# Optimization experiments

Hardware: AMD Instinct MI355X
Metric: run time of the kernel (lower is better)

## Reference

```python
import jax, jax.numpy as jnp
import numpy as np

D_HEAD = 64
SCALE = D_HEAD ** 0.5


def setup_inputs() -> dict:
    key = jax.random.key(0)
    kq, kk, kv = jax.random.split(key, 3)
    shape = (32, 2048, 64)  # (N = batch*heads, HW = seq, C = d_head)
    Q = jax.random.normal(kq, shape, dtype=jnp.float32)
    K = jax.random.normal(kk, shape, dtype=jnp.float32)
    V = jax.random.normal(kv, shape, dtype=jnp.float32)
    return {"Q": Q, "K": K, "V": V}


def reference(Q, K, V):
    # logits = Q K^T / sqrt(d_head); attn = softmax(logits); out = attn V
    logits = jnp.einsum('nqc,nkc->nqk', Q, K) / SCALE  # [N, HW, HW]
    attn = jax.nn.softmax(logits, axis=-1)
    return jnp.einsum('nqk,nkc->nqc', attn, V)  # [N, HW, C]
```

## Files before the change

### kernel.cpp

```cpp
#include <hip/hip_runtime.h>
#include <cstdint>
#include <cstddef>

typedef __bf16 bf16x8 __attribute__((ext_vector_type(8)));
typedef float f32x4 __attribute__((ext_vector_type(4)));
typedef float f32x16 __attribute__((ext_vector_type(16)));
typedef short s16x8 __attribute__((ext_vector_type(8)));
typedef unsigned short u16x4 __attribute__((ext_vector_type(4)));
typedef unsigned short u16x8 __attribute__((ext_vector_type(8)));
typedef int i32x4 __attribute__((ext_vector_type(4)));

#define S_LEN 2048
#define DH    64
#define BK    64
#define NTILE (S_LEN / BK)
#define NH    32

#if __has_builtin(__builtin_amdgcn_exp2f)
#define EXPF(x) __builtin_amdgcn_exp2f(x)
#define QSCALE 0.18033688011112043f
#else
#define EXPF(x) __expf(x)
#define QSCALE 0.125f
#endif

typedef const __attribute__((address_space(1))) void* gas_ptr;
typedef __attribute__((address_space(3))) void* las_ptr;

static __device__ __forceinline__ unsigned short f2bf(float x) {
    unsigned int u = __builtin_bit_cast(unsigned int, x);
    u += 0x7FFFu + ((u >> 16) & 1u);
    return (unsigned short)(u >> 16);
}

static __device__ __forceinline__ unsigned cvtpk(float lo, float hi) {
    unsigned r;
    asm("v_cvt_pk_bf16_f32 %0, %1, %2" : "=v"(r) : "v"(lo), "v"(hi));
    return r;
}

static __device__ __forceinline__ void swap32(int& x, int& y, int hi) {
#if __has_builtin(__builtin_amdgcn_permlane32_swap)
    (void)hi;
    auto r = __builtin_amdgcn_permlane32_swap(x, y, false, false);
    x = r[0]; y = r[1];
#else
    int px = __shfl_xor(x, 32), py = __shfl_xor(y, 32);
    int nx = hi ? py : x;
    int ny = hi ? y  : px;
    x = nx; y = ny;
#endif
}

static __device__ __forceinline__ bf16x8 mkfrag(int lo0, int lo1, int up0, int up1, int hi) {
    swap32(lo0, up0, hi);
    swap32(lo1, up1, hi);
    i32x4 f = {lo0, lo1, up0, up1};
    return __builtin_bit_cast(bf16x8, f);
}

__global__ __launch_bounds__(256) void prepass_kv(
        const float* __restrict__ K, const float* __restrict__ V,
        unsigned short* __restrict__ Kf, unsigned short* __restrict__ Vf)
{
    __shared__ float Tl[64][68];
    const int tid = threadIdx.x;
    const int head = blockIdx.x >> 5;
    const int tile = blockIdx.x & 31;

    const size_t hoff = (size_t)head * S_LEN * DH;
    const size_t soff = hoff + (size_t)tile * 64 * DH;

    #pragma unroll
    for (int p = 0; p < 4; ++p) {
        const int idx = p * 256 + tid;
        const int row = idx >> 4, c4 = idx & 15;
        *(float4*)&Tl[row][c4 * 4] = *(const float4*)(K + soff + (size_t)row * DH + c4 * 4);
    }
    __syncthreads();
    #pragma unroll
    for (int p = 0; p < 2; ++p) {
        const int cid = p * 256 + tid;
        const int sub = cid >> 6;
        const int ln  = cid & 63;
        const int dsub = sub >> 1, half = sub & 1;
        const int row  = half * 32 + (ln & 31);
        const int d0   = dsub * 16 + (ln >> 5) * 8;
        u16x8 o;
        #pragma unroll
        for (int e = 0; e < 8; ++e) o[e] = f2bf(Tl[row][d0 + e]);
        *(u16x8*)&Kf[hoff + (((size_t)tile * 8 + sub) * 64 + ln) * 8] = o;
    }
    __syncthreads();

    #pragma unroll
    for (int p = 0; p < 4; ++p) {
        const int idx = p * 256 + tid;
        const int row = idx >> 4, c4 = idx & 15;
        *(float4*)&Tl[row][c4 * 4] = *(const float4*)(V + soff + (size_t)row * DH + c4 * 4);
    }
    __syncthreads();
    #pragma unroll
    for (int p = 0; p < 2; ++p) {
        const int cid = p * 256 + tid;
        const int sub = cid >> 6;
        const int ln  = cid & 63;
        const int ks = sub >> 1, half = sub & 1;
        const int k0 = ks * 16 + (ln >> 5) * 8;
        const int d  = half * 32 + (ln & 31);
        u16x8 o;
        #pragma unroll
        for (int e = 0; e < 8; ++e) o[e] = f2bf(Tl[k0 + e][d]);
        *(u16x8*)&Vf[hoff + (((size_t)tile * 8 + sub) * 64 + ln) * 8] = o;
    }
}

__global__ __launch_bounds__(512, 4) void sdpa_fused(
        const float* __restrict__ Qg, const unsigned short* __restrict__ Kf,
        const unsigned short* __restrict__ Vf, float* __restrict__ O)
{
    __shared__ __attribute__((aligned(16))) unsigned short SH[32768];

    const int tid = threadIdx.x;
    const int w8  = tid >> 6;
    const int grp = w8 >> 2;
    const int w   = w8 & 3;
    const int ln  = tid & 63;
    const int r31 = ln & 31;
    const int hi  = ln >> 5;

    const int b2 = (blockIdx.x & 7) * 64 + (blockIdx.x >> 3);
    const int n  = b2 >> 4;
    const int qt = b2 & 15;
    const int q0 = qt * 128 + w * 32;

    const size_t hoff = (size_t)n * S_LEN * DH;
    const unsigned short* __restrict__ Kh = Kf + hoff;
    const unsigned short* __restrict__ Vh = Vf + hoff;

    const int kbase = grp * 8192;
    const int vbase = 16384 + grp * 8192;

    s16x8 qf[4];
    {
        const float* Qr = Qg + hoff + (size_t)(q0 + r31) * DH;
        #pragma unroll
        for (int dsub = 0; dsub < 4; ++dsub) {
            const float* s = Qr + dsub * 16 + hi * 8;
            float4 a0 = *(const float4*)s, a1 = *(const float4*)(s + 4);
            s16x8 v;
            v[0] = (short)f2bf(a0.x * QSCALE); v[1] = (short)f2bf(a0.y * QSCALE);
            v[2] = (short)f2bf(a0.z * QSCALE); v[3] = (short)f2bf(a0.w * QSCALE);
            v[4] = (short)f2bf(a1.x * QSCALE); v[5] = (short)f2bf(a1.y * QSCALE);
            v[6] = (short)f2bf(a1.z * QSCALE); v[7] = (short)f2bf(a1.w * QSCALE);
            qf[dsub] = v;
        }
    }

    float l = 0.f;
    f32x16 oacc0 = {}, oacc1 = {};

    auto stage = [&](int buf, int t) {
        #pragma unroll
        for (int pass = 0; pass < 2; ++pass) {
            const int c = pass * 256 + w * 64;
            const unsigned short* gk = Kh + ((size_t)t * 512 + c + ln) * 8;
            __builtin_amdgcn_global_load_lds((gas_ptr)gk,
                    (las_ptr)&SH[kbase + buf * 4096 + c * 8], 16, 0, 0);
            const unsigned short* gv = Vh + ((size_t)t * 512 + c + ln) * 8;
            __builtin_amdgcn_global_load_lds((gas_ptr)gv,
                    (las_ptr)&SH[vbase + buf * 4096 + c * 8], 16, 0, 0);
        }
    };

    const int t0 = grp * (NTILE / 2);

    stage(0, t0);
    __syncthreads();

    auto body = [&](int it, int cur) {
        if (it + 1 < NTILE / 2) stage(cur ^ 1, t0 + it + 1);

        f32x16 s0 = {}, s1 = {};
        __builtin_amdgcn_s_setprio(1);
        #pragma unroll
        for (int dsub = 0; dsub < 4; ++dsub) {
            s16x8 kf0 = *(const s16x8*)&SH[kbase + cur * 4096 + ((dsub * 2 + 0) * 64 + ln) * 8];
            s16x8 kf1 = *(const s16x8*)&SH[kbase + cur * 4096 + ((dsub * 2 + 1) * 64 + ln) * 8];
            s0 = __builtin_amdgcn_mfma_f32_32x32x16_bf16(
                    __builtin_bit_cast(bf16x8, kf0),
                    __builtin_bit_cast(bf16x8, qf[dsub]), s0, 0, 0, 0);
            s1 = __builtin_amdgcn_mfma_f32_32x32x16_bf16(
                    __builtin_bit_cast(bf16x8, kf1),
                    __builtin_bit_cast(bf16x8, qf[dsub]), s1, 0, 0, 0);
        }
        __builtin_amdgcn_s_setprio(0);

        #pragma unroll
        for (int i = 0; i < 16; ++i) {
            s0[i] = EXPF(s0[i]);
            s1[i] = EXPF(s1[i]);
        }
        {
            float a0 = 0.f, a1 = 0.f, a2 = 0.f, a3 = 0.f;
            #pragma unroll
            for (int i = 0; i < 16; i += 4) {
                a0 += s0[i];     a1 += s0[i + 1];
                a2 += s0[i + 2]; a3 += s0[i + 3];
                a0 += s1[i];     a1 += s1[i + 1];
                a2 += s1[i + 2]; a3 += s1[i + 3];
            }
            l += (a0 + a1) + (a2 + a3);
        }

        unsigned wa[8], wb[8];
        #pragma unroll
        for (int i = 0; i < 8; ++i) {
            wa[i] = cvtpk(s0[2 * i], s0[2 * i + 1]);
            wb[i] = cvtpk(s1[2 * i], s1[2 * i + 1]);
        }
        bf16x8 pf[4];
        pf[0] = mkfrag(wa[0], wa[1], wa[2], wa[3], hi);
        pf[1] = mkfrag(wa[4], wa[5], wa[6], wa[7], hi);
        pf[2] = mkfrag(wb[0], wb[1], wb[2], wb[3], hi);
        pf[3] = mkfrag(wb[4], wb[5], wb[6], wb[7], hi);

        __builtin_amdgcn_s_setprio(1);
        #pragma unroll
        for (int ks = 0; ks < 4; ++ks) {
            s16x8 vf0 = *(const s16x8*)&SH[vbase + cur * 4096 + ((ks * 2 + 0) * 64 + ln) * 8];
            s16x8 vf1 = *(const s16x8*)&SH[vbase + cur * 4096 + ((ks * 2 + 1) * 64 + ln) * 8];
            oacc0 = __builtin_amdgcn_mfma_f32_32x32x16_bf16(
                    __builtin_bit_cast(bf16x8, vf0), pf[ks], oacc0, 0, 0, 0);
            oacc1 = __builtin_amdgcn_mfma_f32_32x32x16_bf16(
                    __builtin_bit_cast(bf16x8, vf1), pf[ks], oacc1, 0, 0, 0);
        }
        __builtin_amdgcn_s_setprio(0);

        __syncthreads();
    };

    for (int it = 0; it < NTILE / 2; it += 2) {
        body(it, 0);
        body(it + 1, 1);
    }

    const float lt = l + __shfl_xor(l, 32);

    float* xch = (float*)SH;
    if (grp == 1) {
        float* dst = xch + ((size_t)(w * 64 + ln)) * 34;
        #pragma unroll
        for (int i = 0; i < 16; ++i) {
            dst[i]      = oacc0[i];
            dst[16 + i] = oacc1[i];
        }
        dst[32] = lt;
    }
    __syncthreads();
    if (grp == 0) {
        const float* src = xch + ((size_t)(w * 64 + ln)) * 34;
        const float inv = 1.0f / (lt + src[32]);
        float* Orow = O + hoff + (size_t)(q0 + r31) * DH;
        #pragma unroll
        for (int g = 0; g < 4; ++g) {
            float4 o0 = { (oacc0[4*g]   + src[4*g])     * inv,
                          (oacc0[4*g+1] + src[4*g+1])   * inv,
                          (oacc0[4*g+2] + src[4*g+2])   * inv,
                          (oacc0[4*g+3] + src[4*g+3])   * inv };
            *(float4*)&Orow[g * 8 + hi * 4] = o0;
            float4 o1 = { (oacc1[4*g]   + src[16+4*g])   * inv,
                          (oacc1[4*g+1] + src[16+4*g+1]) * inv,
                          (oacc1[4*g+2] + src[16+4*g+2]) * inv,
                          (oacc1[4*g+3] + src[16+4*g+3]) * inv };
            *(float4*)&Orow[32 + g * 8 + hi * 4] = o1;
        }
    }
}

static __device__ __forceinline__ int swz_fb(int row, int col) {
    return row * 64 + (col ^ ((row & 7) << 3));
}

__global__ __launch_bounds__(256) void sdpa_fwd_fb(
        const float* __restrict__ Q, const float* __restrict__ K,
        const float* __restrict__ V, float* __restrict__ O)
{
    __shared__ __attribute__((aligned(16))) unsigned short Klf[BK * DH];
    __shared__ __attribute__((aligned(16))) unsigned short Vtf[DH * BK];
    __shared__ __attribute__((aligned(16))) unsigned short Plf[4][16 * BK];

    const int tid = threadIdx.x;
    const int w = tid >> 6, ln = tid & 63, lg = ln >> 4, lr = ln & 15;
    const int n = blockIdx.x >> 5, qt = blockIdx.x & 31;
    const int q0 = qt * 64 + w * 16;
    const size_t hoff = (size_t)n * S_LEN * DH;
    const float *Qh = Q + hoff, *Kh = K + hoff, *Vh = V + hoff;
    float* Oh = O + hoff;

    s16x8 qf[2];
    #pragma unroll
    for (int t = 0; t < 2; ++t) {
        const float* src = Qh + (size_t)(q0 + lr) * DH + t * 32 + lg * 8;
        float4 a = *(const float4*)(src);
        float4 b = *(const float4*)(src + 4);
        s16x8 v;
        v[0] = (short)f2bf(a.x * 0.125f); v[1] = (short)f2bf(a.y * 0.125f);
        v[2] = (short)f2bf(a.z * 0.125f); v[3] = (short)f2bf(a.w * 0.125f);
        v[4] = (short)f2bf(b.x * 0.125f); v[5] = (short)f2bf(b.y * 0.125f);
        v[6] = (short)f2bf(b.z * 0.125f); v[7] = (short)f2bf(b.w * 0.125f);
        qf[t] = v;
    }
    float mrow[4] = {-INFINITY, -INFINITY, -INFINITY, -INFINITY};
    float lrow[4] = {0.f, 0.f, 0.f, 0.f};
    f32x4 oacc[4];
    #pragma unroll
    for (int nn = 0; nn < 4; ++nn) oacc[nn] = (f32x4){0.f, 0.f, 0.f, 0.f};

    for (int it = 0; it < NTILE; ++it) {
        const int k0 = it * BK;
        __syncthreads();
        #pragma unroll
        for (int r4 = 0; r4 < 4; ++r4) {
            const int lin = tid + 256 * r4;
            const int row = lin >> 4, c4 = lin & 15;
            float4 kv = *(const float4*)(Kh + (size_t)(k0 + row) * DH + c4 * 4);
            u16x4 kb;
            kb[0] = f2bf(kv.x); kb[1] = f2bf(kv.y); kb[2] = f2bf(kv.z); kb[3] = f2bf(kv.w);
            *(u16x4*)&Klf[swz_fb(row, c4 * 4)] = kb;
            float4 vv = *(const float4*)(Vh + (size_t)(k0 + row) * DH + c4 * 4);
            const float vals[4] = {vv.x, vv.y, vv.z, vv.w};
            #pragma unroll
            for (int ii = 0; ii < 4; ++ii) Vtf[swz_fb(c4 * 4 + ii, row)] = f2bf(vals[ii]);
        }
        __syncthreads();
        f32x4 sacc[4];
        #pragma unroll
        for (int kt = 0; kt < 4; ++kt) {
            f32x4 acc = (f32x4){0.f, 0.f, 0.f, 0.f};
            #pragma unroll
            for (int t = 0; t < 2; ++t) {
                s16x8 kf = *(const s16x8*)&Klf[swz_fb(kt * 16 + lr, t * 32 + lg * 8)];
                acc = __builtin_amdgcn_mfma_f32_16x16x32_bf16(
                        __builtin_bit_cast(bf16x8, qf[t]),
                        __builtin_bit_cast(bf16x8, kf), acc, 0, 0, 0);
            }
            sacc[kt] = acc;
        }
        float alpha[4];
        #pragma unroll
        for (int j = 0; j < 4; ++j) {
            float v = fmaxf(fmaxf(sacc[0][j], sacc[1][j]), fmaxf(sacc[2][j], sacc[3][j]));
            #pragma unroll
            for (int off = 1; off < 16; off <<= 1) v = fmaxf(v, __shfl_xor(v, off));
            const float mn = fmaxf(mrow[j], v);
            alpha[j] = __expf(mrow[j] - mn);
            mrow[j] = mn;
        }
        float psum[4] = {0.f, 0.f, 0.f, 0.f};
        #pragma unroll
        for (int kt = 0; kt < 4; ++kt) {
            #pragma unroll
            for (int j = 0; j < 4; ++j) {
                const float p = __expf(sacc[kt][j] - mrow[j]);
                const unsigned short pb = f2bf(p);
                unsigned int pu = ((unsigned int)pb) << 16;
                psum[j] += __builtin_bit_cast(float, pu);
                Plf[w][swz_fb(lg * 4 + j, kt * 16 + lr)] = pb;
            }
        }
        #pragma unroll
        for (int j = 0; j < 4; ++j) {
            float s = psum[j];
            #pragma unroll
            for (int off = 1; off < 16; off <<= 1) s += __shfl_xor(s, off);
            lrow[j] = lrow[j] * alpha[j] + s;
        }
        #pragma unroll
        for (int nn = 0; nn < 4; ++nn) {
            #pragma unroll
            for (int j = 0; j < 4; ++j) oacc[nn][j] *= alpha[j];
        }
        #pragma unroll
        for (int t = 0; t < 2; ++t) {
            s16x8 pf = *(const s16x8*)&Plf[w][swz_fb(lr, t * 32 + lg * 8)];
            #pragma unroll
            for (int nn = 0; nn < 4; ++nn) {
                s16x8 vf = *(const s16x8*)&Vtf[swz_fb(nn * 16 + lr, t * 32 + lg * 8)];
                oacc[nn] = __builtin_amdgcn_mfma_f32_16x16x32_bf16(
                        __builtin_bit_cast(bf16x8, pf),
                        __builtin_bit_cast(bf16x8, vf), oacc[nn], 0, 0, 0);
            }
        }
    }
    #pragma unroll
    for (int j = 0; j < 4; ++j) {
        const float inv = 1.0f / lrow[j];
        #pragma unroll
        for (int nn = 0; nn < 4; ++nn)
            Oh[(size_t)(q0 + lg * 4 + j) * DH + nn * 16 + lr] = oacc[nn][j] * inv;
    }
}

extern "C" void kernel_launch(void* const* d_in, const int* in_sizes, int n_in,
                              void* d_out, int out_size, void* d_ws, size_t ws_size,
                              hipStream_t stream) {
    const float* Q = (const float*)d_in[0];
    const float* K = (const float*)d_in[1];
    const float* V = (const float*)d_in[2];
    float* O = (float*)d_out;

    const size_t elems    = (size_t)NH * S_LEN * DH;
    const size_t bf_bytes = elems * 2;

    unsigned short* Kf = (unsigned short*)d_ws;
    unsigned short* Vf = Kf + elems;

    if (ws_size >= 2 * bf_bytes) {
        prepass_kv<<<NH * 32, 256, 0, stream>>>(K, V, Kf, Vf);
        sdpa_fused<<<NH * 16, 512, 0, stream>>>(Q, Kf, Vf, O);
    } else {
        sdpa_fwd_fb<<<NH * (S_LEN / 64), 256, 0, stream>>>(Q, K, V, O);
    }
}
```

Baseline: 57.47 us.

## Split K and V staging with vmcnt-based waits for finer-grained prefetch overlap

Splits the per-tile global-to-LDS staging into separate K and V loads. Each is issued right after the matching buffer is consumed, and the full __syncthreads is replaced by partial s_waitcnt vmcnt(2) plus raw s_barrier before each MFMA phase. The aim is to overlap V loads with QK compute and K loads with softmax and PV, instead of draining all memory at one barrier per tile. It adds a second barrier per iteration and relies on exact in-flight load counts for correctness.

```diff
diff --git a/kernel.cpp b/kernel.cpp
--- a/kernel.cpp
+++ b/kernel.cpp
@@ -160,26 +160,34 @@
     float l = 0.f;
     f32x16 oacc0 = {}, oacc1 = {};
 
-    auto stage = [&](int buf, int t) {
+    auto stage_K = [&](int buf, int t) {
         #pragma unroll
         for (int pass = 0; pass < 2; ++pass) {
             const int c = pass * 256 + w * 64;
             const unsigned short* gk = Kh + ((size_t)t * 512 + c + ln) * 8;
             __builtin_amdgcn_global_load_lds((gas_ptr)gk,
                     (las_ptr)&SH[kbase + buf * 4096 + c * 8], 16, 0, 0);
+        }
+    };
+    auto stage_V = [&](int buf, int t) {
+        #pragma unroll
+        for (int pass = 0; pass < 2; ++pass) {
+            const int c = pass * 256 + w * 64;
             const unsigned short* gv = Vh + ((size_t)t * 512 + c + ln) * 8;
             __builtin_amdgcn_global_load_lds((gas_ptr)gv,
                     (las_ptr)&SH[vbase + buf * 4096 + c * 8], 16, 0, 0);
         }
     };
 
-    const int t0 = grp * (NTILE / 2);
-
-    stage(0, t0);
-    __syncthreads();
-
-    auto body = [&](int it, int cur) {
-        if (it + 1 < NTILE / 2) stage(cur ^ 1, t0 + it + 1);
+    const int t0  = grp * (NTILE / 2);
+    const int NT2 = NTILE / 2;
+
+    stage_K(0, t0);
+    stage_V(0, t0);
+
+    auto body = [&](int it, int cur, bool last) {
+        asm volatile("s_waitcnt vmcnt(2)" ::: "memory");
+        __builtin_amdgcn_s_barrier();
 
         f32x16 s0 = {}, s1 = {};
         __builtin_amdgcn_s_setprio(1);
@@ -196,6 +204,8 @@
         }
         __builtin_amdgcn_s_setprio(0);
 
+        if (!last) stage_K(cur ^ 1, t0 + it + 1);
+
         #pragma unroll
         for (int i = 0; i < 16; ++i) {
             s0[i] = EXPF(s0[i]);
@@ -225,6 +235,10 @@
         pf[2] = mkfrag(wb[0], wb[1], wb[2], wb[3], hi);
         pf[3] = mkfrag(wb[4], wb[5], wb[6], wb[7], hi);
 
+        if (last) asm volatile("s_waitcnt vmcnt(0)" ::: "memory");
+        else      asm volatile("s_waitcnt vmcnt(2)" ::: "memory");
+        __builtin_amdgcn_s_barrier();
+
         __builtin_amdgcn_s_setprio(1);
         #pragma unroll
         for (int ks = 0; ks < 4; ++ks) {
@@ -237,16 +251,19 @@
         }
         __builtin_amdgcn_s_setprio(0);
 
-        __syncthreads();
+        if (!last) stage_V(cur ^ 1, t0 + it + 1);
     };
 
-    for (int it = 0; it < NTILE / 2; it += 2) {
-        body(it, 0);
-        body(it + 1, 1);
-    }
+    for (int it = 0; it < NT2 - 2; it += 2) {
+        body(it, 0, false);
+        body(it + 1, 1, false);
+    }
+    body(NT2 - 2, 0, false);
+    body(NT2 - 1, 1, true);
 
     const float lt = l + __shfl_xor(l, 32);
 
+    __syncthreads();
     float* xch = (float*)SH;
     if (grp == 1) {
         float* dst = xch + ((size_t)(w * 64 + ln)) * 34;
```

Measured after the change: 55.95 us. 2.6% less time.
